# Kernel tuning notes

Measured on AMD Instinct MI355X. Metric: run time of the kernel, lower is better.

## Reference

```python
import jax, jax.numpy as jnp
import numpy as np


def conv_t(x, w, stride, padding):
    """torch.nn.functional.conv_transpose2d equivalent.
    w is in torch ConvTranspose2d layout [C_in, C_out, kh, kw]."""
    k = w.shape[2]
    kern = jnp.flip(w, (2, 3)).transpose(1, 0, 2, 3)  # -> OIHW
    pad = k - 1 - padding
    return jax.lax.conv_general_dilated(
        x, kern,
        window_strides=(1, 1),
        padding=[(pad, pad), (pad, pad)],
        lhs_dilation=(stride, stride),
        dimension_numbers=('NCHW', 'OIHW', 'NCHW'))


def setup_inputs() -> dict:
    key = jax.random.key(0)
    ks = jax.random.split(key, 4)
    B, planes, inplanes, H = 32, 256, 128, 28
    x = jax.random.normal(ks[0], (B, planes, H, H), dtype=jnp.float32)
    # torch ConvTranspose2d weight layout: [in, out, kh, kw]
    w_conv2 = jax.random.normal(ks[1], (planes, planes, 3, 3), dtype=jnp.float32) * 0.02
    w_conv1 = jax.random.normal(ks[2], (planes, inplanes, 3, 3), dtype=jnp.float32) * 0.02
    w_up = jax.random.normal(ks[3], (planes // 2, inplanes, 2, 2), dtype=jnp.float32) * 0.02
    # Fixup init: biases zero, scale one
    z = jnp.zeros((1,), dtype=jnp.float32)
    return {
        'x': x, 'w_conv2': w_conv2, 'w_conv1': w_conv1, 'w_up': w_up,
        'bias1a': z, 'bias1b': z, 'bias2a': z, 'bias2b': z,
        'scale': jnp.ones((1,), dtype=jnp.float32),
    }


def reference(x, w_conv2, w_conv1, w_up, bias1a, bias1b, bias2a, bias2b, scale):
    # main branch
    out = conv_t(x + bias1a, w_conv2, stride=1, padding=1)        # [B,planes,H,W]
    out = jax.nn.relu(out + bias1b)
    out = conv_t(out + bias2a, w_conv1, stride=2, padding=1)      # [B,inplanes,2H-1,2W-1]
    out = out * scale + bias2b

    # upsample branch: keep the C/2 channels with the largest (max - min) range,
    # per sample, in ascending-range order (matches np.argsort(diff)[C/2:]).
    C = x.shape[1]
    rng = jnp.max(x, axis=(2, 3)) - jnp.min(x, axis=(2, 3))       # [B,C]
    idx = jnp.argsort(rng, axis=1)[:, C // 2:]                    # [B,C/2]
    x_sel = jnp.take_along_axis(x, idx[:, :, None, None], axis=1)  # [B,C/2,H,W]
    identity = conv_t(x_sel + bias1a, w_up, stride=2, padding=0)  # [B,inplanes,2H,2W]

    # pad main branch top-left by 1 to match 2H x 2W
    out = jnp.pad(out, ((0, 0), (0, 0), (1, 0), (1, 0)))
    out = jax.nn.relu(out + identity)
    return out
```

## Files before the change

### kernel.cpp

```cpp
#include <hip/hip_runtime.h>

#define NB 32
#define NC 256
#define NO 128
#define HH 28
#define HW 784
#define OH 56

typedef unsigned short u16;
typedef __attribute__((ext_vector_type(8))) short bf16x8;
typedef __attribute__((ext_vector_type(4))) float f32x4;
typedef __attribute__((ext_vector_type(8))) unsigned short u16x8;

#define MFMA(A,B,C) __builtin_amdgcn_mfma_f32_16x16x32_bf16(A,B,C,0,0,0)

__device__ __forceinline__ u16 f2bf(float f) {
    unsigned u = __float_as_uint(f);
    unsigned r = (u + 0x7fffu + ((u >> 16) & 1u)) >> 16;
    return (u16)r;
}

__global__ __launch_bounds__(256) void k_prep(
    const float* __restrict__ x, const float* __restrict__ pb1a,
    u16* __restrict__ xT2, float* __restrict__ rng,
    const float* __restrict__ w2, const float* __restrict__ w1,
    const float* __restrict__ wup,
    u16* __restrict__ wT2, u16* __restrict__ wc2T,
    u16* __restrict__ wupT, uint4* __restrict__ r1T4)
{
    __shared__ float sx[8][HW];
    __shared__ float smx[8][4], smn[8][4];

    if (blockIdx.x >= 1024) {
        int blk = blockIdx.x - 1024;
        if (blk < 288) {
            int g = blk * 256 + threadIdx.x;
            int o = g & 255;
            int cb = (g >> 8) & 31;
            int tap = g >> 13;
            int u = 2 - tap / 3, v = 2 - tap % 3;
            u16x8 out;
#pragma unroll
            for (int ci = 0; ci < 8; ++ci) {
                int c = cb * 8 + ci;
                out[ci] = f2bf(w2[((c * NC + o) * 3 + u) * 3 + v]);
            }
            *(u16x8*)(wT2 + (size_t)g * 8) = out;
        } else if (blk < 432) {
            const int taps[9] = {0, 2, 6, 8, 1, 7, 3, 5, 4};
            int g = (blk - 288) * 256 + threadIdx.x;
            int o = g & 127;
            int cb = (g >> 7) & 31;
            int s = g >> 12;
            int tap = taps[s];
            u16x8 out;
#pragma unroll
            for (int ci = 0; ci < 8; ++ci) {
                int c = cb * 8 + ci;
                out[ci] = f2bf(w1[(c * NO + o) * 9 + tap]);
            }
            *(u16x8*)(wc2T + (size_t)g * 8) = out;
        } else if (blk < 464) {
            int g = (blk - 432) * 256 + threadIdx.x;
            int o = g & 127;
            int kb = (g >> 7) & 15;
            int p = g >> 11;
            u16x8 out;
#pragma unroll
            for (int ki = 0; ki < 8; ++ki) {
                int k = kb * 8 + ki;
                out[ki] = f2bf(wup[(k * NO + o) * 4 + p]);
            }
            *(u16x8*)(wupT + (size_t)g * 8) = out;
        } else {
            int g = (blk - 464) * 256 + threadIdx.x;
            int i = g % 176;
            int bc = g / 176;
            int b = bc >> 5, cb = bc & 31;
            int row, cx;
            if (i < 32)      { row = 0;  cx = i; }
            else if (i < 64) { row = 29; cx = i - 32; }
            else {
                int j = i - 64;
                row = 1 + (j >> 2);
                int k = j & 3;
                cx = (k == 0) ? 0 : 28 + k;
            }
            r1T4[((b * 30 + row) * 32 + cb) * 32 + cx] = make_uint4(0, 0, 0, 0);
        }
        return;
    }

    int t = threadIdx.x;
    int b = blockIdx.x >> 5, cb = blockIdx.x & 31;
    float b1a = pb1a[0];
    const float* xb = x + ((size_t)b * NC + cb * 8) * HW;

    float mx[8], mn[8];
#pragma unroll
    for (int ci = 0; ci < 8; ++ci) { mx[ci] = -1e30f; mn[ci] = 1e30f; }
#pragma unroll
    for (int ci = 0; ci < 8; ++ci) {
        const float4* xb4 = (const float4*)(xb + ci * HW);
        float4* sx4 = (float4*)sx[ci];
        if (t < 196) {
            float4 v = xb4[t];
            sx4[t] = v;
            mx[ci] = fmaxf(fmaxf(v.x, v.y), fmaxf(v.z, v.w));
            mn[ci] = fminf(fminf(v.x, v.y), fminf(v.z, v.w));
        }
    }
    int lane = t & 63, wv = t >> 6;
#pragma unroll
    for (int ci = 0; ci < 8; ++ci) {
        float a = mx[ci], i = mn[ci];
        for (int off = 32; off; off >>= 1) {
            a = fmaxf(a, __shfl_down(a, off, 64));
            i = fminf(i, __shfl_down(i, off, 64));
        }
        if (lane == 0) { smx[ci][wv] = a; smn[ci][wv] = i; }
    }
    __syncthreads();
    if (t < 8) {
        float a = fmaxf(fmaxf(smx[t][0], smx[t][1]), fmaxf(smx[t][2], smx[t][3]));
        float i = fminf(fminf(smn[t][0], smn[t][1]), fminf(smn[t][2], smn[t][3]));
        rng[b * NC + cb * 8 + t] = a - i;
    }
    for (int g = t; g < 960; g += 256) {
        int ry = g >> 5, cx = g & 31;
        int y = ry - 1, xx = cx - 1;
        bool valid = (y >= 0 && y < HH && xx >= 0 && xx < HH);
        u16x8 out;
#pragma unroll
        for (int ci = 0; ci < 8; ++ci) {
            float f = valid ? sx[ci][y * 28 + xx] + b1a : 0.f;
            out[ci] = f2bf(f);
        }
        *(u16x8*)(xT2 + ((((size_t)b * 30 + ry) * 32 + cb) * 32 + cx) * 8) = out;
    }
}

__global__ __launch_bounds__(512, 4) void k_conv1x(
    const u16* __restrict__ xT2, const u16* __restrict__ wT2,
    const float* __restrict__ pb1b, const float* __restrict__ pb2a,
    u16* __restrict__ r1T,
    const float* __restrict__ x, const float* __restrict__ rng,
    const float* __restrict__ pb1a, u16* __restrict__ xupT)
{
    __shared__ u16 sA[6 * 16 * 32 * 8];
    if (blockIdx.x >= 448) {
        int blk = blockIdx.x - 448;
        int tid = threadIdx.x;
        int b = blk / 28;
        int qy = blk - b * 28;
        float b1a = pb1a[0];

        float* srng = (float*)sA;
        int* ssel = (int*)(sA + 2048);

        if (tid < 256) srng[tid] = rng[b * NC + tid];
        __syncthreads();
        if (tid < 256) {
            float v = srng[tid];
            int rank = 0;
            for (int j = 0; j < NC; ++j) {
                float u = srng[j];
                rank += (u < v) || (u == v && j < tid);
            }
            if (rank >= NC / 2) ssel[rank - NC / 2] = tid;
        }
        __syncthreads();

        int cx = tid & 31;
        int kb = tid >> 5;
        bool valid = cx < 28;
        const float* xb = x + (size_t)b * NC * HW + qy * 28 + (valid ? cx : 0);
        u16x8 out;
#pragma unroll
        for (int ki = 0; ki < 8; ++ki) {
            int ch = ssel[kb * 8 + ki];
            float f = valid ? xb[ch * HW] + b1a : 0.f;
            out[ki] = f2bf(f);
        }
        size_t g = ((size_t)(b * 28 + qy) * 16 + kb) * 32 + cx;
        *(u16x8*)(xupT + g * 8) = out;
        return;
    }

    int tid = threadIdx.x;
    int wave = tid >> 6, lane = tid & 63;
    int wpi = wave >> 2;
    int wo = wave & 3;
    int l15 = lane & 15, lg = lane >> 4;

    int idx = blockIdx.x;
    int b = idx / 14;
    int rem = idx - b * 14;
    int rg = rem >> 1;
    int og = rem & 1;
    int y0 = rg * 4;

    float b1b = pb1b[0], b2a = pb2a[0];

    int bOff[2];
#pragma unroll
    for (int ot = 0; ot < 2; ++ot)
        bOff[ot] = (lg * 256 + (og * 128 + wo * 32 + ot * 16 + l15)) * 16;

    f32x4 acc[4][2] = {};
    const char* wq = (const char*)wT2;
    const char* ap0 = (const char*)sA;
    const uint4* gx = (const uint4*)xT2;
    uint4* dst = (uint4*)sA;

    int aLane = (2 * wpi) * 8192 + lg * 512 + l15 * 16;

    for (int half = 0; half < 2; ++half) {
        if (half) __syncthreads();
#pragma unroll
        for (int i = 0; i < 6; ++i)
            dst[tid + i * 512] = gx[(b * 30 + y0 + i) * 1024 + half * 512 + tid];
        __syncthreads();

        for (int cc = 0; cc < 128; cc += 32) {
            int c0 = half * 128 + cc;
            int aBase = aLane + cc * 64;
#pragma unroll
            for (int dx = 0; dx < 3; ++dx) {
                bf16x8 w[3][2];
#pragma unroll
                for (int dy = 0; dy < 3; ++dy)
#pragma unroll
                    for (int ot = 0; ot < 2; ++ot)
                        w[dy][ot] = *(const bf16x8*)(wq +
                            (bOff[ot] + (dy * 3 + dx) * 131072 + c0 * 512));
                bf16x8 a[4][2];
#pragma unroll
                for (int r = 0; r < 4; ++r)
#pragma unroll
                    for (int h = 0; h < 2; ++h)
                        a[r][h] = *(const bf16x8*)(ap0 +
                            (aBase + r * 8192 + (h * 16 + dx) * 16));
#pragma unroll
                for (int dy = 0; dy < 3; ++dy)
#pragma unroll
                    for (int m = 0; m < 2; ++m)
#pragma unroll
                        for (int h = 0; h < 2; ++h)
#pragma unroll
                            for (int ot = 0; ot < 2; ++ot)
                                acc[m * 2 + h][ot] =
                                    MFMA(a[m + dy][h], w[dy][ot], acc[m * 2 + h][ot]);
            }
        }
    }

#pragma unroll
    for (int m = 0; m < 2; ++m)
#pragma unroll
        for (int h = 0; h < 2; ++h) {
            int y = y0 + 2 * wpi + m;
            int x0 = h * 16 + lg * 4;
            if (x0 >= 28) continue;
#pragma unroll
            for (int ot = 0; ot < 2; ++ot) {
                int o = og * 128 + wo * 32 + ot * 16 + l15;
                size_t base = ((((size_t)b * 30 + y + 1) * 32 + (o >> 3)) * 32 + (x0 + 1)) * 8 + (o & 7);
#pragma unroll
                for (int r = 0; r < 4; ++r) {
                    float f = fmaxf(acc[m * 2 + h][ot][r] + b1b, 0.f) + b2a;
                    r1T[base + (size_t)r * 8] = f2bf(f);
                }
            }
        }
}

__global__ __launch_bounds__(512, 2) void k_conv2_mfma(
    const u16* __restrict__ r1T, const u16* __restrict__ xupT,
    const u16* __restrict__ wc2T, const u16* __restrict__ wupT,
    const float* __restrict__ pscale, const float* __restrict__ pb2b,
    float* __restrict__ out)
{
    __shared__ uint4 sA2[5120];
    int tid = threadIdx.x;
    int wave = tid >> 6, lane = tid & 63;
    int wpi = wave >> 2;
    int wo = wave & 3;
    int l15 = lane & 15, lg = lane >> 4;

    int b = blockIdx.x / 7;
    int rg = blockIdx.x - b * 7;
    int y0 = rg * 4;

    float scale = pscale[0], b2b = pb2b[0];

    {
        const uint4* src = (const uint4*)(r1T + (size_t)(b * 30 + y0) * 8192);
#pragma unroll
        for (int i = 0; i < 10; ++i)
            sA2[tid + i * 512] = src[tid + i * 512];
    }
    __syncthreads();

    f32x4 acc[4][4][2] = {};

    const char* sp = (const char*)sA2;
    const char* wp = (const char*)wc2T;

    int aBase[4];
#pragma unroll
    for (int pt = 0; pt < 4; ++pt) {
        int rel = 2 * wpi + (pt >> 1) + 1;
        int qt = pt & 1;
        aBase[pt] = ((rel * 32 + lg) * 32 + (qt * 16 + l15 + 1)) * 16;
    }
    int bBase = (lg * 128 + wo * 32 + l15) * 16;

    for (int c0 = 0; c0 < 256; c0 += 32) {
        bf16x8 w[9][2];
#pragma unroll
        for (int s = 0; s < 9; ++s)
#pragma unroll
            for (int ot = 0; ot < 2; ++ot)
                w[s][ot] = *(const bf16x8*)(wp + (bBase + s * 65536 + c0 * 256 + ot * 256));
#pragma unroll
        for (int pt = 0; pt < 4; ++pt) {
            const char* ap = sp + (aBase[pt] + c0 * 64);
            bf16x8 aD = *(const bf16x8*)(ap);
            bf16x8 aC = *(const bf16x8*)(ap - 16);
            bf16x8 aB = *(const bf16x8*)(ap - 16384);
            bf16x8 aA = *(const bf16x8*)(ap - 16400);
#pragma unroll
            for (int ot = 0; ot < 2; ++ot) {
                acc[0][pt][ot] = MFMA(aD, w[0][ot], acc[0][pt][ot]);
                acc[0][pt][ot] = MFMA(aC, w[1][ot], acc[0][pt][ot]);
                acc[0][pt][ot] = MFMA(aB, w[2][ot], acc[0][pt][ot]);
                acc[0][pt][ot] = MFMA(aA, w[3][ot], acc[0][pt][ot]);
                acc[1][pt][ot] = MFMA(aD, w[4][ot], acc[1][pt][ot]);
                acc[1][pt][ot] = MFMA(aB, w[5][ot], acc[1][pt][ot]);
                acc[2][pt][ot] = MFMA(aD, w[6][ot], acc[2][pt][ot]);
                acc[2][pt][ot] = MFMA(aC, w[7][ot], acc[2][pt][ot]);
                acc[3][pt][ot] = MFMA(aD, w[8][ot], acc[3][pt][ot]);
            }
        }
    }

#pragma unroll
    for (int pt = 0; pt < 4; ++pt) {
        int qy = y0 + 2 * wpi + (pt >> 1);
        int qt = pt & 1;
        int qx0 = qt * 16 + lg * 4;
        bool zr = (qy == 0);
#pragma unroll
        for (int ot = 0; ot < 2; ++ot)
#pragma unroll
            for (int r = 0; r < 4; ++r) {
                bool zc = (qx0 + r == 0);
                float a0 = acc[0][pt][ot][r], a1 = acc[1][pt][ot][r];
                float a2 = acc[2][pt][ot][r], a3 = acc[3][pt][ot][r];
                acc[0][pt][ot][r] = (zr || zc) ? 0.f : fmaf(a0, scale, b2b);
                acc[1][pt][ot][r] = zr ? 0.f : fmaf(a1, scale, b2b);
                acc[2][pt][ot][r] = zc ? 0.f : fmaf(a2, scale, b2b);
                acc[3][pt][ot][r] = fmaf(a3, scale, b2b);
            }
    }

    const char* up = (const char*)xupT;
    const char* wu = (const char*)wupT;
    int uBaseA[4];
#pragma unroll
    for (int pt = 0; pt < 4; ++pt) {
        int qy = y0 + 2 * wpi + (pt >> 1);
        int qt = pt & 1;
        uBaseA[pt] = (((b * 28 + qy) * 16 + lg) * 32 + (qt * 16 + l15)) * 16;
    }
    for (int k0 = 0; k0 < 128; k0 += 32) {
        bf16x8 wb[4][2];
#pragma unroll
        for (int p = 0; p < 4; ++p)
#pragma unroll
            for (int ot = 0; ot < 2; ++ot)
                wb[p][ot] = *(const bf16x8*)(wu + (bBase + p * 32768 + k0 * 256 + ot * 256));
#pragma unroll
        for (int pt = 0; pt < 4; ++pt) {
            bf16x8 aU = *(const bf16x8*)(up + (uBaseA[pt] + k0 * 64));
#pragma unroll
            for (int p = 0; p < 4; ++p)
#pragma unroll
                for (int ot = 0; ot < 2; ++ot)
                    acc[p][pt][ot] = MFMA(aU, wb[p][ot], acc[p][pt][ot]);
        }
    }

#pragma unroll
    for (int pt = 0; pt < 4; ++pt) {
        int qy = y0 + 2 * wpi + (pt >> 1);
        int qt = pt & 1;
        int qx0 = qt * 16 + lg * 4;
        if (qx0 >= 28) continue;
#pragma unroll
        for (int ot = 0; ot < 2; ++ot) {
            int o = wo * 32 + ot * 16 + l15;
            size_t base = ((size_t)(b * NO + o) * OH + 2 * qy) * OH + 2 * qx0;
#pragma unroll
            for (int r = 0; r < 4; ++r) {
                float2 v0 = { fmaxf(acc[0][pt][ot][r], 0.f), fmaxf(acc[1][pt][ot][r], 0.f) };
                float2 v1 = { fmaxf(acc[2][pt][ot][r], 0.f), fmaxf(acc[3][pt][ot][r], 0.f) };
                *reinterpret_cast<float2*>(&out[base + 2 * r]) = v0;
                *reinterpret_cast<float2*>(&out[base + OH + 2 * r]) = v1;
            }
        }
    }
}

extern "C" void kernel_launch(void* const* d_in, const int* in_sizes, int n_in,
                              void* d_out, int out_size, void* d_ws, size_t ws_size,
                              hipStream_t stream)
{
    const float* x     = (const float*)d_in[0];
    const float* w2    = (const float*)d_in[1];
    const float* w1    = (const float*)d_in[2];
    const float* wup   = (const float*)d_in[3];
    const float* b1a   = (const float*)d_in[4];
    const float* b1b   = (const float*)d_in[5];
    const float* b2a   = (const float*)d_in[6];
    const float* b2b   = (const float*)d_in[7];
    const float* scale = (const float*)d_in[8];

    char* ws = (char*)d_ws;
    u16* xT2   = (u16*)(ws);
    u16* r1T   = (u16*)(ws + 15728640);
    u16* xupT  = (u16*)(ws + 31457280);
    u16* wT2   = (u16*)(ws + 38797312);
    u16* wc2T  = (u16*)(ws + 39976960);
    u16* wupT  = (u16*)(ws + 40566784);
    float* rng = (float*)(ws + 40697856);
    float* out = (float*)d_out;

    hipLaunchKernelGGL(k_prep, dim3(2192), dim3(256), 0, stream,
                       x, b1a, xT2, rng, w2, w1, wup, wT2, wc2T, wupT, (uint4*)r1T);
    hipLaunchKernelGGL(k_conv1x, dim3(1344), dim3(512), 0, stream,
                       xT2, wT2, b1b, b2a, r1T, x, rng, b1a, xupT);
    hipLaunchKernelGGL(k_conv2_mfma, dim3(NB * 7), dim3(512), 0, stream,
                       r1T, xupT, wc2T, wupT, scale, b2b, out);
}
```

Baseline: 93.01 us.

## Halve conv2 block tile to two rows and stream weights per tap group

The final conv2+upsample kernel now processes 2 output rows per block instead of 4, doubling the grid from 224 to 448 blocks and shrinking shared memory and accumulators. Occupancy hint rises to 3 blocks per CU. The inner loop now loads A fragments once and fetches weights in per-tap-group chunks to cut register pressure. The aim is to fill the 256 CUs better than 224 blocks did, at the cost of less weight reuse per block, so each weight is fetched from global memory twice as often.

```diff
diff --git a/kernel.cpp b/kernel.cpp
--- a/kernel.cpp
+++ b/kernel.cpp
@@ -275,81 +275,117 @@
         }
 }
 
-__global__ __launch_bounds__(512, 2) void k_conv2_mfma(
+__global__ __launch_bounds__(512, 3) void k_conv2_mfma(
     const u16* __restrict__ r1T, const u16* __restrict__ xupT,
     const u16* __restrict__ wc2T, const u16* __restrict__ wupT,
     const float* __restrict__ pscale, const float* __restrict__ pb2b,
     float* __restrict__ out)
 {
-    __shared__ uint4 sA2[5120];
+    __shared__ uint4 sA2[3072];
     int tid = threadIdx.x;
     int wave = tid >> 6, lane = tid & 63;
     int wpi = wave >> 2;
     int wo = wave & 3;
     int l15 = lane & 15, lg = lane >> 4;
 
-    int b = blockIdx.x / 7;
-    int rg = blockIdx.x - b * 7;
-    int y0 = rg * 4;
+    int idx = blockIdx.x;
+    int b = idx / 14;
+    int rg2 = idx - b * 14;
+    int y0 = rg2 * 2;
 
     float scale = pscale[0], b2b = pb2b[0];
 
     {
         const uint4* src = (const uint4*)(r1T + (size_t)(b * 30 + y0) * 8192);
 #pragma unroll
-        for (int i = 0; i < 10; ++i)
+        for (int i = 0; i < 6; ++i)
             sA2[tid + i * 512] = src[tid + i * 512];
     }
     __syncthreads();
 
-    f32x4 acc[4][4][2] = {};
+    f32x4 acc[4][2][2] = {};
 
     const char* sp = (const char*)sA2;
     const char* wp = (const char*)wc2T;
 
-    int aBase[4];
-#pragma unroll
-    for (int pt = 0; pt < 4; ++pt) {
-        int rel = 2 * wpi + (pt >> 1) + 1;
-        int qt = pt & 1;
-        aBase[pt] = ((rel * 32 + lg) * 32 + (qt * 16 + l15 + 1)) * 16;
-    }
+    int aBase[2];
+#pragma unroll
+    for (int pt = 0; pt < 2; ++pt)
+        aBase[pt] = (((wpi + 1) * 32 + lg) * 32 + (pt * 16 + l15 + 1)) * 16;
     int bBase = (lg * 128 + wo * 32 + l15) * 16;
 
     for (int c0 = 0; c0 < 256; c0 += 32) {
-        bf16x8 w[9][2];
-#pragma unroll
-        for (int s = 0; s < 9; ++s)
+        bf16x8 a[2][4];
+#pragma unroll
+        for (int pt = 0; pt < 2; ++pt) {
+            const char* ap = sp + (aBase[pt] + c0 * 64);
+            a[pt][0] = *(const bf16x8*)(ap);
+            a[pt][1] = *(const bf16x8*)(ap - 16);
+            a[pt][2] = *(const bf16x8*)(ap - 16384);
+            a[pt][3] = *(const bf16x8*)(ap - 16400);
+        }
+        {
+            bf16x8 w[4][2];
+#pragma unroll
+            for (int s = 0; s < 4; ++s)
+#pragma unroll
+                for (int ot = 0; ot < 2; ++ot)
+                    w[s][ot] = *(const bf16x8*)(wp + (bBase + s * 65536 + c0 * 256 + ot * 256));
+#pragma unroll
+            for (int pt = 0; pt < 2; ++pt)
+#pragma unroll
+                for (int s = 0; s < 4; ++s)
+#pragma unroll
+                    for (int ot = 0; ot < 2; ++ot)
+                        acc[0][pt][ot] = MFMA(a[pt][s], w[s][ot], acc[0][pt][ot]);
+        }
+        {
+            bf16x8 w[2][2];
+#pragma unroll
+            for (int s = 0; s < 2; ++s)
+#pragma unroll
+                for (int ot = 0; ot < 2; ++ot)
+                    w[s][ot] = *(const bf16x8*)(wp + (bBase + (4 + s) * 65536 + c0 * 256 + ot * 256));
+#pragma unroll
+            for (int pt = 0; pt < 2; ++pt)
+#pragma unroll
+                for (int ot = 0; ot < 2; ++ot) {
+                    acc[1][pt][ot] = MFMA(a[pt][0], w[0][ot], acc[1][pt][ot]);
+                    acc[1][pt][ot] = MFMA(a[pt][2], w[1][ot], acc[1][pt][ot]);
+                }
+        }
+        {
+            bf16x8 w[2][2];
+#pragma unroll
+            for (int s = 0; s < 2; ++s)
+#pragma unroll
+                for (int ot = 0; ot < 2; ++ot)
+                    w[s][ot] = *(const bf16x8*)(wp + (bBase + (6 + s) * 65536 + c0 * 256 + ot * 256));
+#pragma unroll
+            for (int pt = 0; pt < 2; ++pt)
+#pragma unroll
+                for (int ot = 0; ot < 2; ++ot) {
+                    acc[2][pt][ot] = MFMA(a[pt][0], w[0][ot], acc[2][pt][ot]);
+                    acc[2][pt][ot] = MFMA(a[pt][1], w[1][ot], acc[2][pt][ot]);
+                }
+        }
+        {
+            bf16x8 w[2];
 #pragma unroll
             for (int ot = 0; ot < 2; ++ot)
-                w[s][ot] = *(const bf16x8*)(wp + (bBase + s * 65536 + c0 * 256 + ot * 256));
-#pragma unroll
-        for (int pt = 0; pt < 4; ++pt) {
-            const char* ap = sp + (aBase[pt] + c0 * 64);
-            bf16x8 aD = *(const bf16x8*)(ap);
-            bf16x8 aC = *(const bf16x8*)(ap - 16);
-            bf16x8 aB = *(const bf16x8*)(ap - 16384);
-            bf16x8 aA = *(const bf16x8*)(ap - 16400);
-#pragma unroll
-            for (int ot = 0; ot < 2; ++ot) {
-                acc[0][pt][ot] = MFMA(aD, w[0][ot], acc[0][pt][ot]);
-                acc[0][pt][ot] = MFMA(aC, w[1][ot], acc[0][pt][ot]);
-                acc[0][pt][ot] = MFMA(aB, w[2][ot], acc[0][pt][ot]);
-                acc[0][pt][ot] = MFMA(aA, w[3][ot], acc[0][pt][ot]);
-                acc[1][pt][ot] = MFMA(aD, w[4][ot], acc[1][pt][ot]);
-                acc[1][pt][ot] = MFMA(aB, w[5][ot], acc[1][pt][ot]);
-                acc[2][pt][ot] = MFMA(aD, w[6][ot], acc[2][pt][ot]);
-                acc[2][pt][ot] = MFMA(aC, w[7][ot], acc[2][pt][ot]);
-                acc[3][pt][ot] = MFMA(aD, w[8][ot], acc[3][pt][ot]);
-            }
-        }
-    }
-
-#pragma unroll
-    for (int pt = 0; pt < 4; ++pt) {
-        int qy = y0 + 2 * wpi + (pt >> 1);
-        int qt = pt & 1;
-        int qx0 = qt * 16 + lg * 4;
+                w[ot] = *(const bf16x8*)(wp + (bBase + 8 * 65536 + c0 * 256 + ot * 256));
+#pragma unroll
+            for (int pt = 0; pt < 2; ++pt)
+#pragma unroll
+                for (int ot = 0; ot < 2; ++ot)
+                    acc[3][pt][ot] = MFMA(a[pt][0], w[ot], acc[3][pt][ot]);
+        }
+    }
+
+    int qy = y0 + wpi;
+#pragma unroll
+    for (int pt = 0; pt < 2; ++pt) {
+        int qx0 = pt * 16 + lg * 4;
         bool zr = (qy == 0);
 #pragma unroll
         for (int ot = 0; ot < 2; ++ot)
@@ -367,13 +403,10 @@
 
     const char* up = (const char*)xupT;
     const char* wu = (const char*)wupT;
-    int uBaseA[4];
-#pragma unroll
-    for (int pt = 0; pt < 4; ++pt) {
-        int qy = y0 + 2 * wpi + (pt >> 1);
-        int qt = pt & 1;
-        uBaseA[pt] = (((b * 28 + qy) * 16 + lg) * 32 + (qt * 16 + l15)) * 16;
-    }
+    int uBaseA[2];
+#pragma unroll
+    for (int pt = 0; pt < 2; ++pt)
+        uBaseA[pt] = (((b * 28 + qy) * 16 + lg) * 32 + (pt * 16 + l15)) * 16;
     for (int k0 = 0; k0 < 128; k0 += 32) {
         bf16x8 wb[4][2];
 #pragma unroll
@@ -382,7 +415,7 @@
             for (int ot = 0; ot < 2; ++ot)
                 wb[p][ot] = *(const bf16x8*)(wu + (bBase + p * 32768 + k0 * 256 + ot * 256));
 #pragma unroll
-        for (int pt = 0; pt < 4; ++pt) {
+        for (int pt = 0; pt < 2; ++pt) {
             bf16x8 aU = *(const bf16x8*)(up + (uBaseA[pt] + k0 * 64));
 #pragma unroll
             for (int p = 0; p < 4; ++p)
@@ -393,10 +426,8 @@
     }
 
 #pragma unroll
-    for (int pt = 0; pt < 4; ++pt) {
-        int qy = y0 + 2 * wpi + (pt >> 1);
-        int qt = pt & 1;
-        int qx0 = qt * 16 + lg * 4;
+    for (int pt = 0; pt < 2; ++pt) {
+        int qx0 = pt * 16 + lg * 4;
         if (qx0 >= 28) continue;
 #pragma unroll
         for (int ot = 0; ot < 2; ++ot) {
@@ -441,6 +472,6 @@
                        x, b1a, xT2, rng, w2, w1, wup, wT2, wc2T, wupT, (uint4*)r1T);
     hipLaunchKernelGGL(k_conv1x, dim3(1344), dim3(512), 0, stream,
                        xT2, wT2, b1b, b2a, r1T, x, rng, b1a, xupT);
-    hipLaunchKernelGGL(k_conv2_mfma, dim3(NB * 7), dim3(512), 0, stream,
+    hipLaunchKernelGGL(k_conv2_mfma, dim3(448), dim3(512), 0, stream,
                        r1T, xupT, wc2T, wupT, scale, b2b, out);
 }
```

New measurement: 106.7 us. 14.7% more time.
